# Kernel tuning notes

Measured on AMD Instinct MI355X. Metric: run time of the kernel, lower is better.

## Reference

```python
import jax, jax.numpy as jnp
import numpy as np

N, I, O, G = 16384, 128, 128, 16


def setup_inputs() -> dict:
    key = jax.random.key(0)
    k1, k2, k3 = jax.random.split(key, 3)
    coef_norm = np.sqrt(I) * np.sqrt(G)  # smooth_initialization=False
    return {
        "x": jax.random.normal(k1, (N, I), dtype=jnp.float32),
        "cos_amplitudes": jax.random.normal(k2, (O, I, G), dtype=jnp.float32) / coef_norm,
        "sin_amplitudes": jax.random.normal(k3, (O, I, G), dtype=jnp.float32) / coef_norm,
        "bias": jnp.zeros((O,), dtype=jnp.float32),
        "ln_gamma": jnp.ones((O,), dtype=jnp.float32),
        "ln_beta": jnp.zeros((O,), dtype=jnp.float32),
    }


def reference(x, cos_amplitudes, sin_amplitudes, bias, ln_gamma, ln_beta):
    g = cos_amplitudes.shape[-1]
    # frequencies buffer: init_freq_scale=1.0 -> [1, 2, ..., grid_size]
    freqs = jnp.arange(1, g + 1, dtype=x.dtype)  # (G,)
    phases = x[:, :, None] * freqs               # (N, I, G)
    # contraction expressed as a GEMM instead of broadcast-sum over (N,O,I,G)
    out = jnp.einsum("nig,oig->no", jnp.cos(phases), cos_amplitudes)
    out = out + jnp.einsum("nig,oig->no", jnp.sin(phases), sin_amplitudes)
    out = out + bias  # (N, O)
    # LayerNorm over output_dim, eps=1e-5 (torch default)
    mu = jnp.mean(out, axis=-1, keepdims=True)
    var = jnp.var(out, axis=-1, keepdims=True)
    out = (out - mu) / jnp.sqrt(var + 1e-5) * ln_gamma + ln_beta
    return out
```

## Files before the change

### kernel.cpp

```cpp
#include <hip/hip_runtime.h>
#include <hip/hip_bf16.h>
#include <math.h>

#define N_TOK 16384
#define I_DIM 128
#define O_DIM 128
#define G_DIM 16
#define BN 64
#define CI 4
#define KC (CI * G_DIM * 2)
#define NCHUNK (I_DIM / CI)
#define A_STRIDE 136
#define B_STRIDE 136
#define C_STRIDE 132

typedef __bf16 bf16x8 __attribute__((ext_vector_type(8)));
typedef float  f32x4  __attribute__((ext_vector_type(4)));

__global__ __launch_bounds__(256) void fkan_pack_b(
    const float* __restrict__ cosA, const float* __restrict__ sinA,
    __hip_bfloat16* __restrict__ Bp)
{
    int idx = blockIdx.x * 256 + threadIdx.x;
    int kk = idx & 127;
    int o  = (idx >> 7) & 127;
    int c  = idx >> 14;
    int il = kk >> 5;
    int r  = kk & 31;
    int g  = r >> 1;
    int s  = r & 1;
    int i  = c * CI + il;
    const float* src = s ? sinA : cosA;
    float v = src[(o * I_DIM + i) * G_DIM + g];
    Bp[idx] = __float2bfloat16(v);
}

__global__ __launch_bounds__(256) void fkan_main(
    const float* __restrict__ x,
    const __hip_bfloat16* __restrict__ Bp,
    const float* __restrict__ bias,
    const float* __restrict__ gamma,
    const float* __restrict__ beta,
    float* __restrict__ out)
{
    __shared__ __align__(16) __bf16 smem[64 * A_STRIDE + 128 * B_STRIDE];
    __bf16* As = smem;
    __bf16* Bs = smem + 64 * A_STRIDE;
    float*  Cs = (float*)(smem + 64 * A_STRIDE);

    const int t    = threadIdx.x;
    const int lane = t & 63;
    const int wave = t >> 6;
    const int row16 = lane & 15;
    const int quad  = lane >> 4;
    const int n0 = blockIdx.x * BN;

    const int fn  = t >> 2;
    const int fil = t & 3;

    f32x4 acc[4][2];
#pragma unroll
    for (int mt = 0; mt < 4; ++mt)
#pragma unroll
        for (int ot = 0; ot < 2; ++ot)
            acc[mt][ot] = (f32x4){0.f, 0.f, 0.f, 0.f};

    for (int c = 0; c < NCHUNK; ++c) {
        {
            float xv = x[(size_t)(n0 + fn) * I_DIM + (c * CI + fil)];
            float s1, c1;
            __sincosf(xv, &s1, &c1);
            __align__(16) __bf16 feat[32];
            feat[0] = (__bf16)c1;
            feat[1] = (__bf16)s1;
            float ck = c1, sk = s1;
#pragma unroll
            for (int g = 1; g < 16; ++g) {
                float cn = ck * c1 - sk * s1;
                float sn = sk * c1 + ck * s1;
                feat[2 * g]     = (__bf16)cn;
                feat[2 * g + 1] = (__bf16)sn;
                ck = cn; sk = sn;
            }
            bf16x8* dst = (bf16x8*)(As + fn * A_STRIDE + fil * 32);
            const bf16x8* srcv = (const bf16x8*)feat;
#pragma unroll
            for (int j = 0; j < 4; ++j) dst[j] = srcv[j];
        }
        {
            const uint4* src = (const uint4*)(Bp + (size_t)c * (O_DIM * KC));
#pragma unroll
            for (int it = 0; it < 8; ++it) {
                int idx = it * 256 + t;
                uint4 v = src[idx];
                int o    = idx >> 4;
                int kk16 = idx & 15;
                *(uint4*)(Bs + o * B_STRIDE + kk16 * 8) = v;
            }
        }
        __syncthreads();

#pragma unroll
        for (int ks = 0; ks < 4; ++ks) {
            bf16x8 a[4], b[2];
#pragma unroll
            for (int mt = 0; mt < 4; ++mt)
                a[mt] = *(const bf16x8*)(As + (mt * 16 + row16) * A_STRIDE + ks * 32 + quad * 8);
#pragma unroll
            for (int ot = 0; ot < 2; ++ot)
                b[ot] = *(const bf16x8*)(Bs + (wave * 32 + ot * 16 + row16) * B_STRIDE + ks * 32 + quad * 8);
#pragma unroll
            for (int mt = 0; mt < 4; ++mt)
#pragma unroll
                for (int ot = 0; ot < 2; ++ot)
                    acc[mt][ot] = __builtin_amdgcn_mfma_f32_16x16x32_bf16(
                        a[mt], b[ot], acc[mt][ot], 0, 0, 0);
        }
        __syncthreads();
    }

#pragma unroll
    for (int mt = 0; mt < 4; ++mt)
#pragma unroll
        for (int ot = 0; ot < 2; ++ot)
#pragma unroll
            for (int r = 0; r < 4; ++r)
                Cs[(mt * 16 + quad * 4 + r) * C_STRIDE + wave * 32 + ot * 16 + row16] =
                    acc[mt][ot][r];
    __syncthreads();

    {
        const int r  = t >> 2;
        const int qt = t & 3;
        const float* crow = Cs + r * C_STRIDE + qt * 32;
        float vals[32];
        float sum = 0.f, sumsq = 0.f;
#pragma unroll
        for (int j = 0; j < 32; ++j) {
            float v = crow[j] + bias[qt * 32 + j];
            vals[j] = v;
            sum += v;
            sumsq += v * v;
        }
        sum   += __shfl_xor(sum, 1);   sum   += __shfl_xor(sum, 2);
        sumsq += __shfl_xor(sumsq, 1); sumsq += __shfl_xor(sumsq, 2);
        float mu  = sum * (1.0f / O_DIM);
        float var = sumsq * (1.0f / O_DIM) - mu * mu;
        float rstd = rsqrtf(var + 1e-5f);

        float* orow = out + (size_t)(n0 + r) * O_DIM + qt * 32;
#pragma unroll
        for (int jj = 0; jj < 8; ++jj) {
            float4 o4;
            o4.x = (vals[4 * jj + 0] - mu) * rstd * gamma[qt * 32 + 4 * jj + 0] + beta[qt * 32 + 4 * jj + 0];
            o4.y = (vals[4 * jj + 1] - mu) * rstd * gamma[qt * 32 + 4 * jj + 1] + beta[qt * 32 + 4 * jj + 1];
            o4.z = (vals[4 * jj + 2] - mu) * rstd * gamma[qt * 32 + 4 * jj + 2] + beta[qt * 32 + 4 * jj + 2];
            o4.w = (vals[4 * jj + 3] - mu) * rstd * gamma[qt * 32 + 4 * jj + 3] + beta[qt * 32 + 4 * jj + 3];
            *(float4*)(orow + 4 * jj) = o4;
        }
    }
}

extern "C" void kernel_launch(void* const* d_in, const int* in_sizes, int n_in,
                              void* d_out, int out_size, void* d_ws, size_t ws_size,
                              hipStream_t stream) {
    const float* x     = (const float*)d_in[0];
    const float* cosA  = (const float*)d_in[1];
    const float* sinA  = (const float*)d_in[2];
    const float* bias  = (const float*)d_in[3];
    const float* gamma = (const float*)d_in[4];
    const float* beta  = (const float*)d_in[5];
    float* out = (float*)d_out;

    __hip_bfloat16* Bp = (__hip_bfloat16*)d_ws;

    fkan_pack_b<<<dim3((NCHUNK * O_DIM * KC) / 256), dim3(256), 0, stream>>>(cosA, sinA, Bp);
    fkan_main<<<dim3(N_TOK / BN), dim3(256), 0, stream>>>(x, Bp, bias, gamma, beta, out);
}
```

Before: 112.6 us.

## Double-buffer A tiles, load B into registers, use 512-thread blocks

The main kernel now uses 512 threads per block arranged as a 2x4 wave grid. The sincos feature tile A is double-buffered in LDS, so staging the next chunk overlaps the current chunk's MFMAs. The B operand is read directly from global into registers with prefetch, which drops the B LDS tile and one barrier per chunk. The feature work is split across two half-threads that share the rotation recurrence, and the pack kernel is vectorized. This trades more register pressure and setprio and sched_barrier tuning for less LDS traffic and fewer syncs.

Result: slower. 140.6 us (+24.9%).

```diff
diff --git a/kernel.cpp b/kernel.cpp
--- a/kernel.cpp
+++ b/kernel.cpp
@@ -11,7 +11,7 @@
 #define KC (CI * G_DIM * 2)
 #define NCHUNK (I_DIM / CI)
 #define A_STRIDE 136
-#define B_STRIDE 136
+#define ABUF (BN * A_STRIDE)
 #define C_STRIDE 132
 
 typedef __bf16 bf16x8 __attribute__((ext_vector_type(8)));
@@ -19,144 +19,182 @@
 
 __global__ __launch_bounds__(256) void fkan_pack_b(
     const float* __restrict__ cosA, const float* __restrict__ sinA,
-    __hip_bfloat16* __restrict__ Bp)
+    __bf16* __restrict__ Bp)
 {
     int idx = blockIdx.x * 256 + threadIdx.x;
-    int kk = idx & 127;
-    int o  = (idx >> 7) & 127;
-    int c  = idx >> 14;
-    int il = kk >> 5;
-    int r  = kk & 31;
-    int g  = r >> 1;
-    int s  = r & 1;
-    int i  = c * CI + il;
-    const float* src = s ? sinA : cosA;
-    float v = src[(o * I_DIM + i) * G_DIM + g];
-    Bp[idx] = __float2bfloat16(v);
+    int kk8 = idx & 15;
+    int o   = (idx >> 4) & 127;
+    int c   = idx >> 11;
+    int il  = kk8 >> 2;
+    int gq  = kk8 & 3;
+    int i   = c * CI + il;
+    size_t sbase = ((size_t)o * I_DIM + i) * G_DIM + gq * 4;
+    float4 cv = *(const float4*)(cosA + sbase);
+    float4 sv = *(const float4*)(sinA + sbase);
+    bf16x8 v;
+    v[0] = (__bf16)cv.x; v[1] = (__bf16)sv.x;
+    v[2] = (__bf16)cv.y; v[3] = (__bf16)sv.y;
+    v[4] = (__bf16)cv.z; v[5] = (__bf16)sv.z;
+    v[6] = (__bf16)cv.w; v[7] = (__bf16)sv.w;
+    *(bf16x8*)(Bp + (size_t)idx * 8) = v;
 }
 
-__global__ __launch_bounds__(256) void fkan_main(
+__global__ __launch_bounds__(512) void fkan_main(
     const float* __restrict__ x,
-    const __hip_bfloat16* __restrict__ Bp,
+    const __bf16* __restrict__ Bp,
     const float* __restrict__ bias,
     const float* __restrict__ gamma,
     const float* __restrict__ beta,
     float* __restrict__ out)
 {
-    __shared__ __align__(16) __bf16 smem[64 * A_STRIDE + 128 * B_STRIDE];
-    __bf16* As = smem;
-    __bf16* Bs = smem + 64 * A_STRIDE;
-    float*  Cs = (float*)(smem + 64 * A_STRIDE);
-
-    const int t    = threadIdx.x;
-    const int lane = t & 63;
-    const int wave = t >> 6;
+    __shared__ __align__(16) __bf16 smem[2 * ABUF];
+    __bf16* A0 = smem;
+    __bf16* A1 = smem + ABUF;
+
+    const int t     = threadIdx.x;
+    const int lane  = t & 63;
+    const int wave  = t >> 6;
+    const int rg    = wave >> 2;
+    const int cg    = wave & 3;
     const int row16 = lane & 15;
     const int quad  = lane >> 4;
-    const int n0 = blockIdx.x * BN;
-
-    const int fn  = t >> 2;
-    const int fil = t & 3;
-
-    f32x4 acc[4][2];
-#pragma unroll
-    for (int mt = 0; mt < 4; ++mt)
+    const int n0    = blockIdx.x * BN;
+    const int obase = cg * 32 + row16;
+
+    const int srow  = (t & 255) >> 2;
+    const int sil   = t & 3;
+    const int shalf = t >> 8;
+
+    f32x4 acc[2][2];
+#pragma unroll
+    for (int mt = 0; mt < 2; ++mt)
 #pragma unroll
         for (int ot = 0; ot < 2; ++ot)
             acc[mt][ot] = (f32x4){0.f, 0.f, 0.f, 0.f};
 
-    for (int c = 0; c < NCHUNK; ++c) {
-        {
-            float xv = x[(size_t)(n0 + fn) * I_DIM + (c * CI + fil)];
-            float s1, c1;
-            __sincosf(xv, &s1, &c1);
-            __align__(16) __bf16 feat[32];
-            feat[0] = (__bf16)c1;
-            feat[1] = (__bf16)s1;
-            float ck = c1, sk = s1;
-#pragma unroll
-            for (int g = 1; g < 16; ++g) {
-                float cn = ck * c1 - sk * s1;
-                float sn = sk * c1 + ck * s1;
-                feat[2 * g]     = (__bf16)cn;
-                feat[2 * g + 1] = (__bf16)sn;
-                ck = cn; sk = sn;
+    bf16x8 bA[2][4], bB[2][4];
+
+    auto stage_a = [&](int c, __bf16* Ab) {
+        float xv = x[(size_t)(n0 + srow) * I_DIM + (c * CI + sil)];
+        float s1, c1;
+        __sincosf(xv, &s1, &c1);
+        float cb = c1, sb = s1;
+        if (shalf) {
+            float cd = c1, sd = s1;
+#pragma unroll
+            for (int d = 0; d < 3; ++d) {
+                float cn = cd * cd - sd * sd;
+                float sn = 2.f * cd * sd;
+                cd = cn; sd = sn;
             }
-            bf16x8* dst = (bf16x8*)(As + fn * A_STRIDE + fil * 32);
-            const bf16x8* srcv = (const bf16x8*)feat;
-#pragma unroll
-            for (int j = 0; j < 4; ++j) dst[j] = srcv[j];
-        }
-        {
-            const uint4* src = (const uint4*)(Bp + (size_t)c * (O_DIM * KC));
-#pragma unroll
-            for (int it = 0; it < 8; ++it) {
-                int idx = it * 256 + t;
-                uint4 v = src[idx];
-                int o    = idx >> 4;
-                int kk16 = idx & 15;
-                *(uint4*)(Bs + o * B_STRIDE + kk16 * 8) = v;
-            }
-        }
-        __syncthreads();
-
-#pragma unroll
-        for (int ks = 0; ks < 4; ++ks) {
-            bf16x8 a[4], b[2];
-#pragma unroll
-            for (int mt = 0; mt < 4; ++mt)
-                a[mt] = *(const bf16x8*)(As + (mt * 16 + row16) * A_STRIDE + ks * 32 + quad * 8);
-#pragma unroll
-            for (int ot = 0; ot < 2; ++ot)
-                b[ot] = *(const bf16x8*)(Bs + (wave * 32 + ot * 16 + row16) * B_STRIDE + ks * 32 + quad * 8);
-#pragma unroll
-            for (int mt = 0; mt < 4; ++mt)
+            cb = cd * c1 - sd * s1;
+            sb = sd * c1 + cd * s1;
+        }
+        __align__(16) __bf16 feat[16];
+        float cc_ = cb, ss_ = sb;
+#pragma unroll
+        for (int j = 0; j < 8; ++j) {
+            feat[2 * j]     = (__bf16)cc_;
+            feat[2 * j + 1] = (__bf16)ss_;
+            float cn = cc_ * c1 - ss_ * s1;
+            float sn = ss_ * c1 + cc_ * s1;
+            cc_ = cn; ss_ = sn;
+        }
+        bf16x8* dst = (bf16x8*)(Ab + srow * A_STRIDE + sil * 32 + shalf * 16);
+        dst[0] = ((const bf16x8*)feat)[0];
+        dst[1] = ((const bf16x8*)feat)[1];
+    };
+
+    auto load_b = [&](int c, bf16x8 (&b)[2][4]) {
+        const __bf16* p = Bp + (size_t)c * (O_DIM * KC) + (size_t)obase * KC + quad * 8;
+#pragma unroll
+        for (int ot = 0; ot < 2; ++ot)
+#pragma unroll
+            for (int ks = 0; ks < 4; ++ks)
+                b[ot][ks] = *(const bf16x8*)(p + ot * (16 * KC) + ks * 32);
+    };
+
+    auto phase = [&](int c, const __bf16* Ar, __bf16* Aw,
+                     bf16x8 (&bcur)[2][4], bf16x8 (&bnext)[2][4], bool do_next) {
+        bf16x8 a[2][4];
+#pragma unroll
+        for (int mt = 0; mt < 2; ++mt)
+#pragma unroll
+            for (int ks = 0; ks < 4; ++ks)
+                a[mt][ks] = *(const bf16x8*)(Ar + (rg * 32 + mt * 16 + row16) * A_STRIDE
+                                             + ks * 32 + quad * 8);
+        if (do_next) {
+            stage_a(c + 1, Aw);
+            load_b(c + 1, bnext);
+        }
+        asm volatile("s_waitcnt lgkmcnt(0)" ::: "memory");
+        __builtin_amdgcn_sched_barrier(0);
+        __builtin_amdgcn_s_setprio(1);
+#pragma unroll
+        for (int ks = 0; ks < 4; ++ks)
+#pragma unroll
+            for (int mt = 0; mt < 2; ++mt)
 #pragma unroll
                 for (int ot = 0; ot < 2; ++ot)
                     acc[mt][ot] = __builtin_amdgcn_mfma_f32_16x16x32_bf16(
-                        a[mt], b[ot], acc[mt][ot], 0, 0, 0);
-        }
-        __syncthreads();
+                        a[mt][ks], bcur[ot][ks], acc[mt][ot], 0, 0, 0);
+        __builtin_amdgcn_s_setprio(0);
+        __builtin_amdgcn_s_barrier();
+    };
+
+    stage_a(0, A0);
+    load_b(0, bA);
+    asm volatile("s_waitcnt lgkmcnt(0)" ::: "memory");
+    __builtin_amdgcn_s_barrier();
+
+    for (int cc = 0; cc < NCHUNK / 2; ++cc) {
+        phase(2 * cc,     A0, A1, bA, bB, true);
+        phase(2 * cc + 1, A1, A0, bB, bA, cc != NCHUNK / 2 - 1);
     }
 
-#pragma unroll
-    for (int mt = 0; mt < 4; ++mt)
+    float* Cs = (float*)smem;
+#pragma unroll
+    for (int mt = 0; mt < 2; ++mt)
 #pragma unroll
         for (int ot = 0; ot < 2; ++ot)
 #pragma unroll
             for (int r = 0; r < 4; ++r)
-                Cs[(mt * 16 + quad * 4 + r) * C_STRIDE + wave * 32 + ot * 16 + row16] =
-                    acc[mt][ot][r];
+                Cs[(rg * 32 + mt * 16 + quad * 4 + r) * C_STRIDE
+                   + cg * 32 + ot * 16 + row16] = acc[mt][ot][r];
     __syncthreads();
 
     {
-        const int r  = t >> 2;
-        const int qt = t & 3;
-        const float* crow = Cs + r * C_STRIDE + qt * 32;
-        float vals[32];
+        const int r  = t >> 3;
+        const int oc = t & 7;
+        const float* crow = Cs + r * C_STRIDE + oc * 16;
+        float vals[16];
         float sum = 0.f, sumsq = 0.f;
 #pragma unroll
-        for (int j = 0; j < 32; ++j) {
-            float v = crow[j] + bias[qt * 32 + j];
-            vals[j] = v;
-            sum += v;
-            sumsq += v * v;
-        }
-        sum   += __shfl_xor(sum, 1);   sum   += __shfl_xor(sum, 2);
-        sumsq += __shfl_xor(sumsq, 1); sumsq += __shfl_xor(sumsq, 2);
-        float mu  = sum * (1.0f / O_DIM);
-        float var = sumsq * (1.0f / O_DIM) - mu * mu;
+        for (int j4 = 0; j4 < 4; ++j4) {
+            f32x4 v4 = *(const f32x4*)(crow + 4 * j4);
+#pragma unroll
+            for (int e = 0; e < 4; ++e) {
+                float v = v4[e] + bias[oc * 16 + 4 * j4 + e];
+                vals[4 * j4 + e] = v;
+                sum += v;
+                sumsq += v * v;
+            }
+        }
+        sum   += __shfl_xor(sum, 1);   sum   += __shfl_xor(sum, 2);   sum   += __shfl_xor(sum, 4);
+        sumsq += __shfl_xor(sumsq, 1); sumsq += __shfl_xor(sumsq, 2); sumsq += __shfl_xor(sumsq, 4);
+        float mu   = sum * (1.0f / O_DIM);
+        float var  = sumsq * (1.0f / O_DIM) - mu * mu;
         float rstd = rsqrtf(var + 1e-5f);
 
-        float* orow = out + (size_t)(n0 + r) * O_DIM + qt * 32;
-#pragma unroll
-        for (int jj = 0; jj < 8; ++jj) {
+        float* orow = out + (size_t)(n0 + r) * O_DIM + oc * 16;
+#pragma unroll
+        for (int j4 = 0; j4 < 4; ++j4) {
             float4 o4;
-            o4.x = (vals[4 * jj + 0] - mu) * rstd * gamma[qt * 32 + 4 * jj + 0] + beta[qt * 32 + 4 * jj + 0];
-            o4.y = (vals[4 * jj + 1] - mu) * rstd * gamma[qt * 32 + 4 * jj + 1] + beta[qt * 32 + 4 * jj + 1];
-            o4.z = (vals[4 * jj + 2] - mu) * rstd * gamma[qt * 32 + 4 * jj + 2] + beta[qt * 32 + 4 * jj + 2];
-            o4.w = (vals[4 * jj + 3] - mu) * rstd * gamma[qt * 32 + 4 * jj + 3] + beta[qt * 32 + 4 * jj + 3];
-            *(float4*)(orow + 4 * jj) = o4;
+            o4.x = (vals[4*j4+0] - mu) * rstd * gamma[oc*16 + 4*j4+0] + beta[oc*16 + 4*j4+0];
+            o4.y = (vals[4*j4+1] - mu) * rstd * gamma[oc*16 + 4*j4+1] + beta[oc*16 + 4*j4+1];
+            o4.z = (vals[4*j4+2] - mu) * rstd * gamma[oc*16 + 4*j4+2] + beta[oc*16 + 4*j4+2];
+            o4.w = (vals[4*j4+3] - mu) * rstd * gamma[oc*16 + 4*j4+3] + beta[oc*16 + 4*j4+3];
+            *(float4*)(orow + 4 * j4) = o4;
         }
     }
 }
@@ -172,8 +210,8 @@
     const float* beta  = (const float*)d_in[5];
     float* out = (float*)d_out;
 
-    __hip_bfloat16* Bp = (__hip_bfloat16*)d_ws;
-
-    fkan_pack_b<<<dim3((NCHUNK * O_DIM * KC) / 256), dim3(256), 0, stream>>>(cosA, sinA, Bp);
-    fkan_main<<<dim3(N_TOK / BN), dim3(256), 0, stream>>>(x, Bp, bias, gamma, beta, out);
+    __bf16* Bp = (__bf16*)d_ws;
+
+    fkan_pack_b<<<dim3((NCHUNK * O_DIM * KC) / 8 / 256), dim3(256), 0, stream>>>(cosA, sinA, Bp);
+    fkan_main<<<dim3(N_TOK / BN), dim3(512), 0, stream>>>(x, Bp, bias, gamma, beta, out);
 }
```

## Prepack B into MFMA fragment order and double-buffer A with register prefetch

Applied to the files above, without the earlier changes.

The pack kernel now writes the weights directly in per-lane MFMA fragment layout with vectorized float4 reads and 16-byte writes. The main kernel loads B fragments straight from global memory into registers, one chunk ahead, so B no longer goes through shared memory. The A feature tile is double-buffered in LDS, with the x load two chunks ahead, which drops to one barrier per chunk and raises wave priority around the MFMAs. The cost is more register pressure, since two sets of B fragments are held, and B is read from global or L2 by every block without LDS reuse.

Measured after the change: 104.5 us. 7.2% less time.

```diff
diff --git a/kernel.cpp b/kernel.cpp
--- a/kernel.cpp
+++ b/kernel.cpp
@@ -11,7 +11,7 @@
 #define KC (CI * G_DIM * 2)
 #define NCHUNK (I_DIM / CI)
 #define A_STRIDE 136
-#define B_STRIDE 136
+#define ABUF (BN * A_STRIDE)
 #define C_STRIDE 132
 
 typedef __bf16 bf16x8 __attribute__((ext_vector_type(8)));
@@ -19,41 +19,45 @@
 
 __global__ __launch_bounds__(256) void fkan_pack_b(
     const float* __restrict__ cosA, const float* __restrict__ sinA,
-    __hip_bfloat16* __restrict__ Bp)
+    __bf16* __restrict__ Bp)
 {
-    int idx = blockIdx.x * 256 + threadIdx.x;
-    int kk = idx & 127;
-    int o  = (idx >> 7) & 127;
-    int c  = idx >> 14;
-    int il = kk >> 5;
-    int r  = kk & 31;
-    int g  = r >> 1;
-    int s  = r & 1;
-    int i  = c * CI + il;
-    const float* src = s ? sinA : cosA;
-    float v = src[(o * I_DIM + i) * G_DIM + g];
-    Bp[idx] = __float2bfloat16(v);
+    int tid = blockIdx.x * 256 + threadIdx.x;
+    int gq  = tid & 3;
+    int i   = (tid >> 2) & 127;
+    int o   = tid >> 9;
+    int c   = i >> 2, ks = i & 3;
+    int cg  = o >> 5, ot = (o >> 4) & 1, row16 = o & 15;
+    int lane = gq * 16 + row16;
+    size_t sbase = ((size_t)o * I_DIM + i) * G_DIM + gq * 4;
+    float4 cv = *(const float4*)(cosA + sbase);
+    float4 sv = *(const float4*)(sinA + sbase);
+    bf16x8 v;
+    v[0] = (__bf16)cv.x; v[1] = (__bf16)sv.x;
+    v[2] = (__bf16)cv.y; v[3] = (__bf16)sv.y;
+    v[4] = (__bf16)cv.z; v[5] = (__bf16)sv.z;
+    v[6] = (__bf16)cv.w; v[7] = (__bf16)sv.w;
+    size_t frag = (((size_t)c * 4 + cg) * 4 + ks) * 2 + ot;
+    *(bf16x8*)(Bp + (frag * 64 + lane) * 8) = v;
 }
 
 __global__ __launch_bounds__(256) void fkan_main(
     const float* __restrict__ x,
-    const __hip_bfloat16* __restrict__ Bp,
+    const __bf16* __restrict__ Bp,
     const float* __restrict__ bias,
     const float* __restrict__ gamma,
     const float* __restrict__ beta,
     float* __restrict__ out)
 {
-    __shared__ __align__(16) __bf16 smem[64 * A_STRIDE + 128 * B_STRIDE];
-    __bf16* As = smem;
-    __bf16* Bs = smem + 64 * A_STRIDE;
-    float*  Cs = (float*)(smem + 64 * A_STRIDE);
-
-    const int t    = threadIdx.x;
-    const int lane = t & 63;
-    const int wave = t >> 6;
+    __shared__ __align__(16) __bf16 smem[2 * ABUF];
+    __bf16* A0 = smem;
+    __bf16* A1 = smem + ABUF;
+
+    const int t     = threadIdx.x;
+    const int lane  = t & 63;
+    const int cg    = t >> 6;
     const int row16 = lane & 15;
     const int quad  = lane >> 4;
-    const int n0 = blockIdx.x * BN;
+    const int n0    = blockIdx.x * BN;
 
     const int fn  = t >> 2;
     const int fil = t & 3;
@@ -65,67 +69,91 @@
         for (int ot = 0; ot < 2; ++ot)
             acc[mt][ot] = (f32x4){0.f, 0.f, 0.f, 0.f};
 
-    for (int c = 0; c < NCHUNK; ++c) {
-        {
-            float xv = x[(size_t)(n0 + fn) * I_DIM + (c * CI + fil)];
-            float s1, c1;
-            __sincosf(xv, &s1, &c1);
-            __align__(16) __bf16 feat[32];
-            feat[0] = (__bf16)c1;
-            feat[1] = (__bf16)s1;
-            float ck = c1, sk = s1;
-#pragma unroll
-            for (int g = 1; g < 16; ++g) {
-                float cn = ck * c1 - sk * s1;
-                float sn = sk * c1 + ck * s1;
-                feat[2 * g]     = (__bf16)cn;
-                feat[2 * g + 1] = (__bf16)sn;
-                ck = cn; sk = sn;
+    bf16x8 bA[2][4], bB[2][4];
+
+    auto ld_x = [&](int c) -> float {
+        return x[(size_t)(n0 + fn) * I_DIM + c * CI + fil];
+    };
+
+    auto ld_b = [&](int c, bf16x8 (&b)[2][4]) {
+        const bf16x8* base = (const bf16x8*)Bp + ((size_t)(c * 4 + cg) * 8) * 64 + lane;
+#pragma unroll
+        for (int ks = 0; ks < 4; ++ks)
+#pragma unroll
+            for (int ot = 0; ot < 2; ++ot)
+                b[ot][ks] = base[(ks * 2 + ot) * 64];
+    };
+
+    auto stage_a = [&](float xv, __bf16* Ab) {
+        float s1, c1;
+        __sincosf(xv, &s1, &c1);
+        __align__(16) __bf16 feat[32];
+        feat[0] = (__bf16)c1;
+        feat[1] = (__bf16)s1;
+        float ck = c1, sk = s1;
+#pragma unroll
+        for (int g = 1; g < 16; ++g) {
+            float cn = ck * c1 - sk * s1;
+            float sn = sk * c1 + ck * s1;
+            feat[2 * g]     = (__bf16)cn;
+            feat[2 * g + 1] = (__bf16)sn;
+            ck = cn; sk = sn;
+        }
+        bf16x8* dst = (bf16x8*)(Ab + fn * A_STRIDE + fil * 32);
+        const bf16x8* srcv = (const bf16x8*)feat;
+#pragma unroll
+        for (int j = 0; j < 4; ++j) dst[j] = srcv[j];
+    };
+
+    auto phase = [&](int c, const __bf16* Ar, __bf16* Aw,
+                     bf16x8 (&bcur)[2][4], bf16x8 (&bnext)[2][4], float xs, float& xn) {
+        const bool pf = (c + 1 < NCHUNK);
+        if (pf) ld_b(c + 1, bnext);
+        if (c + 2 < NCHUNK) xn = ld_x(c + 2);
+        if (pf) stage_a(xs, Aw);
+
+        __builtin_amdgcn_s_setprio(1);
+#pragma unroll
+        for (int ks = 0; ks < 4; ++ks) {
+            bf16x8 a[4];
+#pragma unroll
+            for (int mt = 0; mt < 4; ++mt)
+                a[mt] = *(const bf16x8*)(Ar + (mt * 16 + row16) * A_STRIDE
+                                         + ks * 32 + quad * 8);
+#pragma unroll
+            for (int mt = 0; mt < 4; ++mt) {
+                acc[mt][0] = __builtin_amdgcn_mfma_f32_16x16x32_bf16(a[mt], bcur[0][ks], acc[mt][0], 0, 0, 0);
+                acc[mt][1] = __builtin_amdgcn_mfma_f32_16x16x32_bf16(a[mt], bcur[1][ks], acc[mt][1], 0, 0, 0);
             }
-            bf16x8* dst = (bf16x8*)(As + fn * A_STRIDE + fil * 32);
-            const bf16x8* srcv = (const bf16x8*)feat;
-#pragma unroll
-            for (int j = 0; j < 4; ++j) dst[j] = srcv[j];
-        }
-        {
-            const uint4* src = (const uint4*)(Bp + (size_t)c * (O_DIM * KC));
-#pragma unroll
-            for (int it = 0; it < 8; ++it) {
-                int idx = it * 256 + t;
-                uint4 v = src[idx];
-                int o    = idx >> 4;
-                int kk16 = idx & 15;
-                *(uint4*)(Bs + o * B_STRIDE + kk16 * 8) = v;
-            }
-        }
-        __syncthreads();
-
-#pragma unroll
-        for (int ks = 0; ks < 4; ++ks) {
-            bf16x8 a[4], b[2];
-#pragma unroll
-            for (int mt = 0; mt < 4; ++mt)
-                a[mt] = *(const bf16x8*)(As + (mt * 16 + row16) * A_STRIDE + ks * 32 + quad * 8);
-#pragma unroll
-            for (int ot = 0; ot < 2; ++ot)
-                b[ot] = *(const bf16x8*)(Bs + (wave * 32 + ot * 16 + row16) * B_STRIDE + ks * 32 + quad * 8);
-#pragma unroll
-            for (int mt = 0; mt < 4; ++mt)
-#pragma unroll
-                for (int ot = 0; ot < 2; ++ot)
-                    acc[mt][ot] = __builtin_amdgcn_mfma_f32_16x16x32_bf16(
-                        a[mt], b[ot], acc[mt][ot], 0, 0, 0);
-        }
-        __syncthreads();
+        }
+        __builtin_amdgcn_s_setprio(0);
+
+        asm volatile("s_waitcnt lgkmcnt(0)" ::: "memory");
+        __builtin_amdgcn_sched_barrier(0);
+        __builtin_amdgcn_s_barrier();
+    };
+
+    float xA = ld_x(0);
+    float xB;
+    ld_b(0, bA);
+    stage_a(xA, A0);
+    xB = ld_x(1);
+    asm volatile("s_waitcnt lgkmcnt(0)" ::: "memory");
+    __builtin_amdgcn_s_barrier();
+
+    for (int cc = 0; cc < NCHUNK / 2; ++cc) {
+        phase(2 * cc,     A0, A1, bA, bB, xB, xA);
+        phase(2 * cc + 1, A1, A0, bB, bA, xA, xB);
     }
 
+    float* Cs = (float*)smem;
 #pragma unroll
     for (int mt = 0; mt < 4; ++mt)
 #pragma unroll
         for (int ot = 0; ot < 2; ++ot)
 #pragma unroll
             for (int r = 0; r < 4; ++r)
-                Cs[(mt * 16 + quad * 4 + r) * C_STRIDE + wave * 32 + ot * 16 + row16] =
+                Cs[(mt * 16 + quad * 4 + r) * C_STRIDE + cg * 32 + ot * 16 + row16] =
                     acc[mt][ot][r];
     __syncthreads();
 
@@ -136,27 +164,31 @@
         float vals[32];
         float sum = 0.f, sumsq = 0.f;
 #pragma unroll
-        for (int j = 0; j < 32; ++j) {
-            float v = crow[j] + bias[qt * 32 + j];
-            vals[j] = v;
-            sum += v;
-            sumsq += v * v;
+        for (int j4 = 0; j4 < 8; ++j4) {
+            f32x4 v4 = *(const f32x4*)(crow + 4 * j4);
+#pragma unroll
+            for (int e = 0; e < 4; ++e) {
+                float v = v4[e] + bias[qt * 32 + 4 * j4 + e];
+                vals[4 * j4 + e] = v;
+                sum += v;
+                sumsq += v * v;
+            }
         }
         sum   += __shfl_xor(sum, 1);   sum   += __shfl_xor(sum, 2);
         sumsq += __shfl_xor(sumsq, 1); sumsq += __shfl_xor(sumsq, 2);
-        float mu  = sum * (1.0f / O_DIM);
-        float var = sumsq * (1.0f / O_DIM) - mu * mu;
+        float mu   = sum * (1.0f / O_DIM);
+        float var  = sumsq * (1.0f / O_DIM) - mu * mu;
         float rstd = rsqrtf(var + 1e-5f);
 
         float* orow = out + (size_t)(n0 + r) * O_DIM + qt * 32;
 #pragma unroll
-        for (int jj = 0; jj < 8; ++jj) {
+        for (int j4 = 0; j4 < 8; ++j4) {
             float4 o4;
-            o4.x = (vals[4 * jj + 0] - mu) * rstd * gamma[qt * 32 + 4 * jj + 0] + beta[qt * 32 + 4 * jj + 0];
-            o4.y = (vals[4 * jj + 1] - mu) * rstd * gamma[qt * 32 + 4 * jj + 1] + beta[qt * 32 + 4 * jj + 1];
-            o4.z = (vals[4 * jj + 2] - mu) * rstd * gamma[qt * 32 + 4 * jj + 2] + beta[qt * 32 + 4 * jj + 2];
-            o4.w = (vals[4 * jj + 3] - mu) * rstd * gamma[qt * 32 + 4 * jj + 3] + beta[qt * 32 + 4 * jj + 3];
-            *(float4*)(orow + 4 * jj) = o4;
+            o4.x = (vals[4*j4+0] - mu) * rstd * gamma[qt*32 + 4*j4+0] + beta[qt*32 + 4*j4+0];
+            o4.y = (vals[4*j4+1] - mu) * rstd * gamma[qt*32 + 4*j4+1] + beta[qt*32 + 4*j4+1];
+            o4.z = (vals[4*j4+2] - mu) * rstd * gamma[qt*32 + 4*j4+2] + beta[qt*32 + 4*j4+2];
+            o4.w = (vals[4*j4+3] - mu) * rstd * gamma[qt*32 + 4*j4+3] + beta[qt*32 + 4*j4+3];
+            *(float4*)(orow + 4 * j4) = o4;
         }
     }
 }
@@ -172,8 +204,8 @@
     const float* beta  = (const float*)d_in[5];
     float* out = (float*)d_out;
 
-    __hip_bfloat16* Bp = (__hip_bfloat16*)d_ws;
-
-    fkan_pack_b<<<dim3((NCHUNK * O_DIM * KC) / 256), dim3(256), 0, stream>>>(cosA, sinA, Bp);
+    __bf16* Bp = (__bf16*)d_ws;
+
+    fkan_pack_b<<<dim3((NCHUNK * O_DIM * KC) / 8 / 256), dim3(256), 0, stream>>>(cosA, sinA, Bp);
     fkan_main<<<dim3(N_TOK / BN), dim3(256), 0, stream>>>(x, Bp, bias, gamma, beta, out);
 }
```
